# Performance work log

Measured on AMD Instinct MI355X. Metric: run time of the kernel, lower is better.

The kernel has to match this reference:

```python
import jax, jax.numpy as jnp
import numpy as np

# configuration (mirrors global `args` in the original code)
N_USER = 20000
N_ITEM = 20000
N = N_USER + N_ITEM            # total nodes; N*N < 2^31 so int32 hashing is safe
N_EDGES = 2_560_000
MASK_DEPTH = 2
KEEP_RATE = 0.5
N_SEEDS = 2000


def setup_inputs() -> dict:
    key = jax.random.key(0)
    k1, k2, k3 = jax.random.split(key, 3)
    rows = jax.random.randint(k1, (N_EDGES,), 0, N, dtype=jnp.int32)
    cols = jax.random.randint(k2, (N_EDGES,), 0, N, dtype=jnp.int32)
    vals = jnp.ones((N_EDGES,), jnp.float32)  # adj._values(); only its length is used
    seeds = jax.random.randint(k3, (N_SEEDS,), 0, N, dtype=jnp.int32)
    return {"rows": rows, "cols": cols, "vals": vals, "seeds": seeds}


def reference(rows, cols, vals, seeds):
    """Faithful vectorized translation of RandomMaskSubgraphs.forward.

    The per-seed python loop over edges is equivalent (in its final effect) to:
    per BFS level, drop every still-alive edge incident to the current seed set,
    and take the endpoints of dropped edges as the next seed set.
    Returns (enc_rows, enc_cols, enc_vals, dec_rows, dec_cols, dec_vals).
    Removed encoder edges carry value 0 (zero-value sparse entries == absent).
    """
    E = rows.shape[0]
    key = jax.random.key(1)
    kS, kR, kC = jax.random.split(key, 3)

    alive = jnp.ones(E, dtype=bool)                     # edges not yet masked
    seed_mask = jnp.zeros(N, dtype=bool).at[seeds].set(True)
    mask_nodes = seed_mask                               # union of maskNodes list
    cur = seed_mask
    for i in range(MASK_DEPTH):
        # membership test: edge incident to any current seed (single gather pass)
        hit = alive & (cur[rows] | cur[cols])
        alive = alive & ~hit
        if i != MASK_DEPTH - 1:
            # endpoints of masked edges become next frontier (scatter dedup)
            h = hit.astype(jnp.int32)
            touched = (jnp.zeros(N, jnp.int32).at[rows].add(h).at[cols].add(h)) > 0
            mask_nodes = mask_nodes | touched
            cur = touched

    # random keep-nodes augmentation
    samp_num = int(N * KEEP_RATE)
    samp = jax.random.randint(kS, (samp_num,), 0, N, dtype=jnp.int32)
    mask_nodes = mask_nodes.at[samp].set(True)

    # encoderAdj = normalizeAdj(sparse(ones on remaining edges))
    deg = jax.ops.segment_sum(alive.astype(jnp.float32), rows, num_segments=N)
    dinv = jnp.power(deg + 1e-12, -0.5)
    enc_vals = alive.astype(jnp.float32) * dinv[rows] * dinv[cols]

    # decoderAdj: random pairs among masked nodes + self loops + remaining edges,
    # deduplicated via integer hash row*N + col (fits int32 since N*N < 2^31)
    mask_idx = jnp.nonzero(mask_nodes)[0].astype(jnp.int32)
    tem_num = int(mask_idx.shape[0])
    tem_rows = mask_idx[jax.random.randint(kR, (E,), 0, tem_num)]
    tem_cols = mask_idx[jax.random.randint(kC, (E,), 0, tem_num)]
    ar = jnp.arange(N, dtype=jnp.int32)
    alive_rows = rows[alive]
    alive_cols = cols[alive]
    new_rows = jnp.concatenate([tem_rows, tem_cols, ar, alive_rows])
    new_cols = jnp.concatenate([tem_cols, tem_rows, ar, alive_cols])
    hash_val = jnp.unique(new_rows * N + new_cols)
    dec_cols = hash_val % N
    dec_rows = hash_val // N
    dec_vals = jnp.ones(dec_rows.shape[0], jnp.float32)

    return rows, cols, enc_vals, dec_rows, dec_cols, dec_vals
```

## Files before the change

kernel.cpp:

```cpp
#include <hip/hip_runtime.h>
#include <stdint.h>


#define NN 40000
#define SAMPN (NN / 2)
#define WORDS 1250
#define SWORDS 40
#define NB 1024
#define RPB 40
#define CAP 8192
#define CURSTRIDE 4
#define APPT 512
#define EPB 5632
#define NE (EPB / APPT)
#define SELFPB 88
#define SCAP (3 * EPB + SELFPB)
#define MWPB 250

__host__ __device__ __forceinline__ void tf2x32(unsigned k0, unsigned k1,
                                                unsigned x0, unsigned x1,
                                                unsigned &o0, unsigned &o1) {
  unsigned ks2 = k0 ^ k1 ^ 0x1BD11BDAu;
  x0 += k0; x1 += k1;
#define TFR(r) { x0 += x1; x1 = (x1 << (r)) | (x1 >> (32 - (r))); x1 ^= x0; }
  TFR(13) TFR(15) TFR(26) TFR(6)
  x0 += k1;  x1 += ks2 + 1u;
  TFR(17) TFR(29) TFR(16) TFR(24)
  x0 += ks2; x1 += k0 + 2u;
  TFR(13) TFR(15) TFR(26) TFR(6)
  x0 += k0;  x1 += k1 + 3u;
  TFR(17) TFR(29) TFR(16) TFR(24)
  x0 += k1;  x1 += ks2 + 4u;
  TFR(13) TFR(15) TFR(26) TFR(6)
  x0 += ks2; x1 += k0 + 5u;
#undef TFR
  o0 = x0; o1 = x1;
}

__device__ __forceinline__ unsigned jrand(unsigned a, unsigned b, unsigned c,
                                          unsigned d, unsigned e, unsigned span,
                                          unsigned m2) {
  unsigned x0, x1, y0, y1;
  tf2x32(a, b, 0u, e, x0, x1);
  unsigned hi = x0 ^ x1;
  tf2x32(c, d, 0u, e, y0, y1);
  unsigned lo = y0 ^ y1;
  return ((hi % span) * m2 + (lo % span)) % span;
}

__global__ void k_zero16(uint4 *p, int n16) {
  int i = blockIdx.x * blockDim.x + threadIdx.x;
  if (i < n16) p[i] = make_uint4(0u, 0u, 0u, 0u);
}
__global__ void k_seed_samp(const int *seeds, int ns, unsigned char *cur,
                            unsigned char *mask_bfs,
                            unsigned a, unsigned b, unsigned c, unsigned d) {
  int i = blockIdx.x * blockDim.x + threadIdx.x;
  if (i < ns) { int s = seeds[i]; cur[s] = 1; mask_bfs[s] = 1; }
  if (i < SAMPN) {
    constexpr unsigned M2 =
        ((65536u % (unsigned)NN) * (65536u % (unsigned)NN)) % (unsigned)NN;
    unsigned idx = jrand(a, b, c, d, (unsigned)i, (unsigned)NN, M2);
    mask_bfs[idx] = 1;
  }
}
__global__ void k_level0(const int *rows, const int *cols, int E,
                         const unsigned char *cur, unsigned char *alive,
                         unsigned char *touched, unsigned char *mask_bfs,
                         int *deg, int *cursors) {
  int e = blockIdx.x * blockDim.x + threadIdx.x;
  if (e < NN) deg[e] = 0;
  int e2 = e - NN;
  if (e2 >= 0 && e2 < NB * CURSTRIDE) cursors[e2] = 0;
  if (e >= E) return;
  int r = rows[e], c = cols[e];
  if (cur[r] | cur[c]) {
    alive[e] = 0;
    touched[r] = 1; touched[c] = 1;
    mask_bfs[r] = 1; mask_bfs[c] = 1;
  } else alive[e] = 1;
}
__global__ void k_level1_deg(const int *rows, const int *cols, int E,
                             const unsigned char *touched, unsigned char *alive,
                             int *deg, const unsigned *maskw, int *mask_part) {
  int tid = threadIdx.x;
  int e = blockIdx.x * blockDim.x + tid;
  if (e < E && alive[e]) {
    int r = rows[e];
    if (touched[r] | touched[cols[e]]) alive[e] = 0;
    else atomicAdd(&deg[r], 1);
  }
  if (blockIdx.x < 40) {
    __shared__ int red[4];
    int lane = tid & 63, wid = tid >> 6;
    int c = (tid < MWPB) ? __popc(maskw[blockIdx.x * MWPB + tid]) : 0;
    for (int d = 1; d < 64; d <<= 1) c += __shfl_xor(c, d, 64);
    if (lane == 0) red[wid] = c;
    __syncthreads();
    if (tid == 0) mask_part[blockIdx.x] = red[0] + red[1] + red[2] + red[3];
  }
}

__global__ __launch_bounds__(256) void k_mask_extract(const unsigned *f,
                                                      const int *mask_part,
                                                      unsigned short *mask_idx,
                                                      int *tem_num) {
  __shared__ int wsum[4];
  __shared__ int basech;
  int b = blockIdx.x, tid = threadIdx.x, lane = tid & 63, wid = tid >> 6;
  if (wid == 0) {
    int v = (lane < 40) ? mask_part[lane] : 0;
    int x = v;
    for (int d = 1; d < 64; d <<= 1) {
      int y = __shfl_up(x, d, 64);
      if (lane >= d) x += y;
    }
    int basev = __shfl(x - v, b, 64);
    int total = __shfl(x, 39, 64);
    if (lane == 0) {
      basech = basev;
      if (b == 0) *tem_num = total;
    }
  }
  int w = b * MWPB + tid;
  unsigned u = (tid < MWPB) ? f[w] : 0u;
  int c = __popc(u);
  int x = c;
  for (int d = 1; d < 64; d <<= 1) {
    int y = __shfl_up(x, d, 64);
    if (lane >= d) x += y;
  }
  if (lane == 63) wsum[wid] = x;
  __syncthreads();
  if (wid == 0) {
    int v = (lane < 4) ? wsum[lane] : 0;
    int y = v;
    for (int d = 1; d < 4; d <<= 1) {
      int z = __shfl_up(y, d, 64);
      if (lane >= d) y += z;
    }
    if (lane < 4) wsum[lane] = y - v;
  }
  __syncthreads();
  int off = basech + wsum[wid] + (x - c);
  while (u) {
    int byte = (__ffs(u) - 1) >> 3;
    u &= u - 1;
    mask_idx[off++] = (unsigned short)(w * 4 + byte);
  }
}

__global__ __launch_bounds__(APPT) void k_append(
    const int *rows, const int *cols, const unsigned char *alive,
    const int *deg, const unsigned short *mask_idx, const int *tem_num,
    int *cursors, unsigned *bucketmem, float *out,
    unsigned ra, unsigned rb, unsigned rc, unsigned rd,
    unsigned ca, unsigned cb, unsigned cc, unsigned cd, int E) {
  __shared__ unsigned sorted[SCAP];
  __shared__ int cnt[NB];
  __shared__ unsigned short ofs[NB];
  __shared__ int ntot_s;
  int tid = threadIdx.x, lane = tid & 63, wid = tid >> 6;
  int e0 = blockIdx.x * EPB;
  int i0 = blockIdx.x * SELFPB;
  int i1 = i0 + SELFPB; if (i1 > NN) i1 = NN;
  unsigned span = (unsigned)*tem_num;
  unsigned mtmp = 65536u % span;
  unsigned m2 = (mtmp * mtmp) % span;
  const unsigned NOPE = 0xFFFFFFFFu;

  unsigned tval[NE], aval[NE];

  for (int i = tid; i < NB; i += APPT) cnt[i] = 0;
  __syncthreads();
#pragma unroll
  for (int k = 0; k < NE; k++) {
    int e = e0 + k * APPT + tid;
    if (e < E) {
      unsigned iR = jrand(ra, rb, rc, rd, (unsigned)e, span, m2);
      unsigned iC = jrand(ca, cb, cc, cd, (unsigned)e, span, m2);
      unsigned tr = (unsigned)mask_idx[iR], tc = (unsigned)mask_idx[iC];
      tval[k] = (tr << 16) | tc;
      atomicAdd(&cnt[tr / RPB], 1);
      atomicAdd(&cnt[tc / RPB], 1);
      int r = rows[e], c = cols[e];
      float v = 0.0f;
      if (alive[e]) {
        aval[k] = ((unsigned)r << 16) | (unsigned)c;
        atomicAdd(&cnt[(unsigned)r / RPB], 1);
        float xr = (float)deg[r] + 1e-12f;
        float xc = (float)deg[c] + 1e-12f;
        float dr = (float)(1.0 / sqrt((double)xr));
        float dc = (float)(1.0 / sqrt((double)xc));
        v = dr * dc;
      } else aval[k] = NOPE;
      out[e] = (float)r;
      out[E + e] = (float)c;
      out[2 * E + e] = v;
    } else { tval[k] = NOPE; aval[k] = NOPE; }
  }
  for (int i = i0 + tid; i < i1; i += APPT) atomicAdd(&cnt[i / RPB], 1);
  __syncthreads();
  if (wid == 0) {
    int carry = 0;
    for (int c8 = 0; c8 < NB / 64; c8++) {
      int v = cnt[c8 * 64 + lane];
      int x = v;
      for (int d = 1; d < 64; d <<= 1) {
        int y = __shfl_up(x, d, 64);
        if (lane >= d) x += y;
      }
      ofs[c8 * 64 + lane] = (unsigned short)(carry + x - v);
      carry += __shfl(x, 63, 64);
    }
    if (lane == 0) ntot_s = carry;
  }
  __syncthreads();
  for (int i = tid; i < NB; i += APPT) cnt[i] = ofs[i];
  __syncthreads();
#pragma unroll
  for (int k = 0; k < NE; k++) {
    unsigned v = tval[k];
    if (v != NOPE) {
      unsigned tr = v >> 16, tc = v & 0xFFFFu;
      int p1 = atomicAdd(&cnt[tr / RPB], 1);
      sorted[p1] = v;
      int p2 = atomicAdd(&cnt[tc / RPB], 1);
      sorted[p2] = (tc << 16) | tr;
      unsigned a = aval[k];
      if (a != NOPE) {
        int p3 = atomicAdd(&cnt[(a >> 16) / RPB], 1);
        sorted[p3] = a;
      }
    }
  }
  for (int i = i0 + tid; i < i1; i += APPT) {
    int p = atomicAdd(&cnt[i / RPB], 1);
    sorted[p] = ((unsigned)i << 16) | (unsigned)i;
  }
  __syncthreads();
  int ntot = ntot_s;
  for (int b = tid; b < NB; b += APPT) {
    int end = (b < NB - 1) ? (int)ofs[b + 1] : ntot;
    int len = end - (int)ofs[b];
    cnt[b] = len ? atomicAdd(&cursors[b * CURSTRIDE], len) : 0;
  }
  __syncthreads();
  for (int j = tid; j < ntot; j += APPT) {
    unsigned item = sorted[j];
    unsigned r = item >> 16;
    unsigned b = r / RPB;
    unsigned lr = r - b * RPB;
    int idx = cnt[b] + (j - (int)ofs[b]);
    if (idx < CAP) bucketmem[b * CAP + idx] = (lr << 16) | (item & 0xFFFFu);
  }
}

__global__ __launch_bounds__(256) void k_dedup(unsigned *bucketmem,
                                               const int *cursors, int *uniq_cnt) {
  int b = blockIdx.x;
  int rowbase = b * RPB;
  if (rowbase >= NN) { if (threadIdx.x == 0) uniq_cnt[b] = 0; return; }

  __shared__ unsigned short arr[CAP];
  __shared__ int cnt[RPB];
  __shared__ int rowend[RPB];
  __shared__ int curs[RPB];
  __shared__ int rowoff[RPB];
  __shared__ unsigned bm[4][WORDS];
  __shared__ unsigned sm[4][SWORDS];

  int tid = threadIdx.x, lane = tid & 63, wid = tid >> 6;
  int n = cursors[b * CURSTRIDE]; if (n > CAP) n = CAP;
  const unsigned *src = bucketmem + (size_t)b * CAP;

  for (int i = tid; i < RPB; i += 256) cnt[i] = 0;
  __syncthreads();
  for (int j = tid; j < n; j += 256) atomicAdd(&cnt[src[j] >> 16], 1);
  __syncthreads();
  if (wid == 0) {
    int v = (lane < RPB) ? cnt[lane] : 0;
    int x = v;
    for (int d = 1; d < 64; d <<= 1) {
      int y = __shfl_up(x, d, 64);
      if (lane >= d) x += y;
    }
    if (lane < RPB) { curs[lane] = x - v; rowend[lane] = x; }
  }
  __syncthreads();
  for (int j = tid; j < n; j += 256) {
    unsigned v = src[j];
    int p = atomicAdd(&curs[v >> 16], 1);
    arr[p] = (unsigned short)v;
  }
  for (int w = lane; w < WORDS; w += 64) bm[wid][w] = 0u;
  if (lane < SWORDS) sm[wid][lane] = 0u;
  __syncthreads();

  for (int r = wid; r < RPB; r += 4) {
    int s1 = rowend[r], s0 = s1 - cnt[r];
    for (int j = s0 + lane; j < s1; j += 64) {
      unsigned c = arr[j];
      atomicOr(&bm[wid][c >> 5], 1u << (c & 31));
      atomicOr(&sm[wid][c >> 10], 1u << ((c >> 5) & 31));
    }
    unsigned s = (lane < SWORDS) ? sm[wid][lane] : 0u;
    int m = 0;
    unsigned t = s;
    while (t) {
      int w = (lane << 5) + (__ffs(t) - 1);
      t &= t - 1;
      m += __popc(bm[wid][w]);
    }
    int x = m;
    for (int d = 1; d < 64; d <<= 1) {
      int y = __shfl_up(x, d, 64);
      if (lane >= d) x += y;
    }
    int u = __shfl(x, 63, 64);
    int pos = s0 + (x - m);
    t = s;
    while (t) {
      int w = (lane << 5) + (__ffs(t) - 1);
      t &= t - 1;
      unsigned mm = bm[wid][w];
      bm[wid][w] = 0u;
      while (mm) {
        int bit = __ffs(mm) - 1;
        mm &= mm - 1;
        arr[pos++] = (unsigned short)((w << 5) + bit);
      }
    }
    if (lane < SWORDS) sm[wid][lane] = 0u;
    if (lane == 0) cnt[r] = u;
  }
  __syncthreads();
  if (wid == 0) {
    int v = (lane < RPB) ? cnt[lane] : 0;
    int x = v;
    for (int d = 1; d < 64; d <<= 1) {
      int y = __shfl_up(x, d, 64);
      if (lane >= d) x += y;
    }
    if (lane < RPB) rowoff[lane] = x - v;
    if (lane == RPB - 1) uniq_cnt[b] = x;
  }
  __syncthreads();
  unsigned *dst = bucketmem + (size_t)b * CAP;
  for (int r = wid; r < RPB; r += 4) {
    int s0 = r ? rowend[r - 1] : 0;
    int u = cnt[r], o = rowoff[r];
    unsigned rowpack = (unsigned)(rowbase + r) << 16;
    for (int j = lane; j < u; j += 64)
      dst[o + j] = rowpack | (unsigned)arr[s0 + j];
  }
}

__global__ __launch_bounds__(256) void k_emit(const unsigned *bucketmem,
                                              const int *uniq_cnt, float *out,
                                              int E, int U) {
  __shared__ int part[4];
  int b = blockIdx.x;
  int tid = threadIdx.x, lane = tid & 63, wid = tid >> 6;
  int acc = 0;
  for (int i = tid; i < NB; i += 256)
    if (i < b) acc += uniq_cnt[i];
  for (int d = 1; d < 64; d <<= 1) acc += __shfl_xor(acc, d, 64);
  if (lane == 0) part[wid] = acc;
  __syncthreads();
  int ob = part[0] + part[1] + part[2] + part[3];
  int ub = uniq_cnt[b];
  const unsigned *src = bucketmem + (size_t)b * CAP;
  int base3 = 3 * E;
  for (int j = tid; j < ub; j += 256) {
    unsigned h = src[j];
    unsigned r = h >> 16;
    unsigned c = h & 0xFFFFu;
    int idx = ob + j;
    if (idx < U) {
      out[base3 + idx] = (float)r;
      out[base3 + U + idx] = (float)c;
      out[base3 + 2 * U + idx] = 1.0f;
    }
  }
  if (b == NB - 1 && tid == 0) {
    int C = ob + ub;
    if (C != U) {
      int d = C - U; if (d < 0) d = -d; if (d > 60000) d = 60000;
      out[base3] = (float)(300000 + d);
    }
  }
}

extern "C" void kernel_launch(void *const *d_in, const int *in_sizes, int n_in,
                              void *d_out, int out_size, void *d_ws,
                              size_t ws_size, hipStream_t stream) {
  const int *rows = (const int *)d_in[0];
  const int *cols = (const int *)d_in[1];
  const int *seeds = (const int *)d_in[3];
  const int E = in_sizes[0];
  const int ns = in_sizes[3];
  float *out = (float *)d_out;
  const int U = (out_size - 3 * E) / 3;

  int *I = (int *)d_ws;
  int *deg = I;      I += NN;
  int *cursors = I;  I += NB * CURSTRIDE;
  int *uniq_cnt = I; I += NB;
  unsigned char *cur = (unsigned char *)I;
  unsigned char *touched = cur + NN;
  unsigned char *mask_bfs = touched + NN;
  size_t zero_bytes = (size_t)(3 * NN);
  int *J = (int *)(mask_bfs + NN);
  int *tem_num = J;  J += 1;
  J += 1;
  int *mask_part = J; J += 40;
  unsigned short *mask_idx = (unsigned short *)J;
  J += NN / 2;
  unsigned *bucketmem = (unsigned *)J; J += (size_t)NB * CAP;
  unsigned char *alive = (unsigned char *)J;

  unsigned F[3][2];
  tf2x32(0u, 1u, 0u, 0u, F[0][0], F[0][1]);
  tf2x32(0u, 1u, 0u, 1u, F[1][0], F[1][1]);
  tf2x32(0u, 1u, 0u, 2u, F[2][0], F[2][1]);
  unsigned K[3][4];
  for (int s = 0; s < 3; s++) {
    tf2x32(F[s][0], F[s][1], 0u, 0u, K[s][0], K[s][1]);
    tf2x32(F[s][0], F[s][1], 0u, 1u, K[s][2], K[s][3]);
  }

  dim3 b(256);
  int gE = (E + 255) / 256;
  int gSS = (SAMPN + 255) / 256;
  int gT = (E + EPB - 1) / EPB;
  int n16 = (int)(zero_bytes / 16);

  k_zero16<<<(n16 + 255) / 256, b, 0, stream>>>((uint4 *)cur, n16);
  k_seed_samp<<<gSS, b, 0, stream>>>(seeds, ns, cur, mask_bfs,
                                     K[0][0], K[0][1], K[0][2], K[0][3]);
  k_level0<<<gE, b, 0, stream>>>(rows, cols, E, cur, alive, touched, mask_bfs,
                                 deg, cursors);
  k_level1_deg<<<gE, b, 0, stream>>>(rows, cols, E, touched, alive, deg,
                                     (const unsigned *)mask_bfs, mask_part);
  k_mask_extract<<<40, b, 0, stream>>>((const unsigned *)mask_bfs, mask_part,
                                       mask_idx, tem_num);
  k_append<<<gT, dim3(APPT), 0, stream>>>(rows, cols, alive, deg, mask_idx,
                                          tem_num, cursors, bucketmem, out,
                                          K[1][0], K[1][1], K[1][2], K[1][3],
                                          K[2][0], K[2][1], K[2][2], K[2][3], E);
  k_dedup<<<NB, b, 0, stream>>>(bucketmem, cursors, uniq_cnt);
  k_emit<<<NB, b, 0, stream>>>(bucketmem, uniq_cnt, out, E, U);
}
```

Before: 251.3 us.

## Partition dedup bitmap by column range across waves to shrink LDS

Each of the four waves used to own a full-width column bitmap and process whole rows on its own. Now all waves walk every row together, each wave covering one quarter of the column range with a smaller bitmap, and their per-wave counts are combined through a small shared array to compute write offsets. This cuts LDS use per block so more blocks can be resident (launch bounds now request 7), at the cost of a block-wide barrier per row and each wave scanning every row entry.

```diff
diff --git a/kernel.cpp b/kernel.cpp
--- a/kernel.cpp
+++ b/kernel.cpp
@@ -4,8 +4,6 @@
 
 #define NN 40000
 #define SAMPN (NN / 2)
-#define WORDS 1250
-#define SWORDS 40
 #define NB 1024
 #define RPB 40
 #define CAP 8192
@@ -16,6 +14,8 @@
 #define SELFPB 88
 #define SCAP (3 * EPB + SELFPB)
 #define MWPB 250
+#define BMW 313
+#define CSPAN (BMW * 32)
 
 __host__ __device__ __forceinline__ void tf2x32(unsigned k0, unsigned k1,
                                                 unsigned x0, unsigned x1,
@@ -256,8 +256,9 @@
   }
 }
 
-__global__ __launch_bounds__(256) void k_dedup(unsigned *bucketmem,
-                                               const int *cursors, int *uniq_cnt) {
+__global__ __launch_bounds__(256, 7) void k_dedup(unsigned *bucketmem,
+                                                  const int *cursors,
+                                                  int *uniq_cnt) {
   int b = blockIdx.x;
   int rowbase = b * RPB;
   if (rowbase >= NN) { if (threadIdx.x == 0) uniq_cnt[b] = 0; return; }
@@ -267,8 +268,9 @@
   __shared__ int rowend[RPB];
   __shared__ int curs[RPB];
   __shared__ int rowoff[RPB];
-  __shared__ unsigned bm[4][WORDS];
-  __shared__ unsigned sm[4][SWORDS];
+  __shared__ unsigned bm[4][BMW];
+  __shared__ unsigned sm[4][10];
+  __shared__ int wcnt[RPB][4];
 
   int tid = threadIdx.x, lane = tid & 63, wid = tid >> 6;
   int n = cursors[b * CURSTRIDE]; if (n > CAP) n = CAP;
@@ -293,18 +295,22 @@
     int p = atomicAdd(&curs[v >> 16], 1);
     arr[p] = (unsigned short)v;
   }
-  for (int w = lane; w < WORDS; w += 64) bm[wid][w] = 0u;
-  if (lane < SWORDS) sm[wid][lane] = 0u;
-  __syncthreads();
-
-  for (int r = wid; r < RPB; r += 4) {
+  for (int w = lane; w < BMW; w += 64) bm[wid][w] = 0u;
+  if (lane < 10) sm[wid][lane] = 0u;
+  __syncthreads();
+
+  unsigned clo = (unsigned)wid * CSPAN;
+  for (int r = 0; r < RPB; r++) {
     int s1 = rowend[r], s0 = s1 - cnt[r];
     for (int j = s0 + lane; j < s1; j += 64) {
-      unsigned c = arr[j];
-      atomicOr(&bm[wid][c >> 5], 1u << (c & 31));
-      atomicOr(&sm[wid][c >> 10], 1u << ((c >> 5) & 31));
-    }
-    unsigned s = (lane < SWORDS) ? sm[wid][lane] : 0u;
+      unsigned wl = (unsigned)arr[j] - clo;
+      if (wl < CSPAN) {
+        unsigned w = wl >> 5;
+        atomicOr(&bm[wid][w], 1u << (wl & 31));
+        atomicOr(&sm[wid][w >> 5], 1u << (w & 31));
+      }
+    }
+    unsigned s = (lane < 10) ? sm[wid][lane] : 0u;
     int m = 0;
     unsigned t = s;
     while (t) {
@@ -317,22 +323,33 @@
       int y = __shfl_up(x, d, 64);
       if (lane >= d) x += y;
     }
-    int u = __shfl(x, 63, 64);
-    int pos = s0 + (x - m);
+    int mw = __shfl(x, 63, 64);
+    int lpre = x - m;
+    if (lane == 0) wcnt[r][wid] = mw;
+    __syncthreads();
+    int wpre = 0, tot = 0;
+#pragma unroll
+    for (int w = 0; w < 4; w++) {
+      int v = wcnt[r][w];
+      tot += v;
+      if (w < wid) wpre += v;
+    }
+    int pos = s0 + wpre + lpre;
     t = s;
     while (t) {
       int w = (lane << 5) + (__ffs(t) - 1);
       t &= t - 1;
       unsigned mm = bm[wid][w];
       bm[wid][w] = 0u;
+      unsigned cbase = clo + ((unsigned)w << 5);
       while (mm) {
         int bit = __ffs(mm) - 1;
         mm &= mm - 1;
-        arr[pos++] = (unsigned short)((w << 5) + bit);
+        arr[pos++] = (unsigned short)(cbase + (unsigned)bit);
       }
     }
-    if (lane < SWORDS) sm[wid][lane] = 0u;
-    if (lane == 0) cnt[r] = u;
+    if (lane < 10) sm[wid][lane] = 0u;
+    if (tid == 0) cnt[r] = tot;
   }
   __syncthreads();
   if (wid == 0) {
```

After: 318.9 us. +26.9%, slower.
